# Kernel optimization log

Measured on AMD Instinct MI355X. Metric: run time of the kernel, lower is better.

The kernel has to match this reference:

```python
import jax, jax.numpy as jnp
import numpy as np

B, S, D, H, E, TOP_K = 8, 2048, 2048, 2048, 4, 2


def setup_inputs() -> dict:
    key = jax.random.key(0)
    ks = jax.random.split(key, 6)
    scale = 0.02
    return {
        "hidden_states": jax.random.normal(ks[0], (B, S, D), jnp.float32),
        "gate_w": jax.random.normal(ks[1], (E, D), jnp.float32) * scale,  # Linear(D -> E), no bias
        "w1": jax.random.normal(ks[2], (E, D, H), jnp.float32) * scale,   # per-expert Linear(D -> H)
        "b1": jnp.zeros((E, H), jnp.float32),
        "w2": jax.random.normal(ks[3], (E, H, H), jnp.float32) * scale,   # per-expert Linear(H -> H)
        "b2": jnp.zeros((E, H), jnp.float32),
    }


def reference(hidden_states, gate_w, w1, b1, w2, b2):
    b, s, d = hidden_states.shape
    x = hidden_states.reshape(-1, d)                       # [N, D]
    n = x.shape[0]

    # Router: softmax in fp32, top-k, renormalize (matches torch forward)
    logits = jnp.einsum("nd,ed->ne", x, gate_w)            # [N, E]
    rw = jax.nn.softmax(logits.astype(jnp.float32), axis=-1)
    top_w, sel = jax.lax.top_k(rw, TOP_K)                  # [N, K]
    top_w = top_w / jnp.sum(top_w, axis=-1, keepdims=True)
    top_w = top_w.astype(x.dtype)

    # Scatter top-k weights back to a dense [N, E] combine matrix
    w_full = jnp.zeros((n, E), x.dtype).at[jnp.arange(n)[:, None], sel].set(top_w)

    # Per-expert FFN: Linear -> exact GELU -> Linear (dense over all tokens,
    # combined with zero weight for unselected experts == gather/scatter math)
    h1 = jax.nn.gelu(jnp.einsum("nd,edh->enh", x, w1) + b1[:, None, :], approximate=False)
    out_e = jnp.einsum("enh,eho->eno", h1, w2) + b2[:, None, :]  # [E, N, H]

    out = jnp.einsum("eno,ne->no", out_e, w_full)          # weighted combine
    return out.reshape(b, s, -1)
```

## Files before the change

### kernel.cpp

```cpp
#include <hip/hip_runtime.h>
#include <hip/hip_bf16.h>
#include <math.h>

typedef __bf16 bf16x8 __attribute__((ext_vector_type(8)));
typedef __bf16 bf16x4 __attribute__((ext_vector_type(4)));
typedef float f32x4 __attribute__((ext_vector_type(4)));

typedef __attribute__((address_space(1))) void GV;
typedef __attribute__((address_space(3))) void LV;

template <int OSTRIDE, bool EBLOCK>
__global__ __launch_bounds__(256) void transpose_cvt(const float* __restrict__ in,
                                                     __bf16* __restrict__ out) {
  __shared__ float tile[32][33];
  const int e = blockIdx.z;
  const size_t ibase = (size_t)e * 2048 * 2048;
  const size_t obase = EBLOCK ? (size_t)e * 2048 * 2048 : (size_t)e * 2048;
  int c0 = blockIdx.x * 32, r0 = blockIdx.y * 32;
  int tx = threadIdx.x & 31, ty = threadIdx.x >> 5;
#pragma unroll
  for (int i = 0; i < 32; i += 8)
    tile[ty + i][tx] = in[ibase + (size_t)(r0 + ty + i) * 2048 + c0 + tx];
  __syncthreads();
#pragma unroll
  for (int i = 0; i < 32; i += 8)
    out[obase + (size_t)(c0 + ty + i) * OSTRIDE + r0 + tx] = (__bf16)tile[tx][ty + i];
}

__global__ __launch_bounds__(256) void router_kernel(const float* __restrict__ x,
                                                     const float* __restrict__ gw,
                                                     float* __restrict__ comb,
                                                     int* __restrict__ pairid,
                                                     int* __restrict__ cnt) {
  int lane = threadIdx.x & 63;
  int wv = threadIdx.x >> 6;
  int n = blockIdx.x * 4 + wv;
  const float* xr = x + (size_t)n * 2048;
  float s0 = 0.f, s1 = 0.f, s2 = 0.f, s3 = 0.f;
  for (int d = lane; d < 2048; d += 64) {
    float xv = xr[d];
    s0 += xv * gw[d];
    s1 += xv * gw[2048 + d];
    s2 += xv * gw[4096 + d];
    s3 += xv * gw[6144 + d];
  }
#pragma unroll
  for (int off = 32; off > 0; off >>= 1) {
    s0 += __shfl_down(s0, off);
    s1 += __shfl_down(s1, off);
    s2 += __shfl_down(s2, off);
    s3 += __shfl_down(s3, off);
  }
  if (lane == 0) {
    float l[4] = {s0, s1, s2, s3};
    float m = fmaxf(fmaxf(l[0], l[1]), fmaxf(l[2], l[3]));
    float p[4], sum = 0.f;
#pragma unroll
    for (int e = 0; e < 4; ++e) { p[e] = expf(l[e] - m); sum += p[e]; }
#pragma unroll
    for (int e = 0; e < 4; ++e) p[e] /= sum;
    int i1 = 0;
#pragma unroll
    for (int e = 1; e < 4; ++e) if (p[e] > p[i1]) i1 = e;
    int i2 = -1;
#pragma unroll
    for (int e = 0; e < 4; ++e) {
      if (e == i1) continue;
      if (i2 < 0 || p[e] > p[i2]) i2 = e;
    }
    float ws = p[i1] + p[i2];
#pragma unroll
    for (int e = 0; e < 4; ++e)
      comb[(size_t)n * 4 + e] = (e == i1 || e == i2) ? p[e] / ws : 0.f;
    int a = min(i1, i2), b = max(i1, i2);
    int pid = (a == 0) ? (b - 1) : ((a == 1) ? (1 + b) : (2 + b));
    pairid[n] = pid;
    atomicAdd(&cnt[pid], 1);
  }
}

__global__ void scan6(const int* __restrict__ cnt, int* __restrict__ off) {
  int o = 0;
  for (int i = 0; i < 6; ++i) { off[i] = o; o += cnt[i]; }
}

__global__ __launch_bounds__(256) void assign_kernel(const int* __restrict__ pairid,
                                                     const float4* __restrict__ comb4,
                                                     const int* __restrict__ off,
                                                     int* __restrict__ cur,
                                                     int* __restrict__ perm,
                                                     float4* __restrict__ comb_s,
                                                     int* __restrict__ pm_s) {
  int n = blockIdx.x * 256 + threadIdx.x;
  int pid = pairid[n];
  int pos = off[pid] + atomicAdd(&cur[pid], 1);
  perm[pos] = n;
  comb_s[pos] = comb4[n];
  const int lut[6] = {3, 5, 9, 6, 10, 12};
  pm_s[pos] = lut[pid];
}

__global__ __launch_bounds__(256) void cvt_gather(const float4* __restrict__ hs,
                                                  const int* __restrict__ perm,
                                                  bf16x4* __restrict__ xb) {
  int pos = blockIdx.x;
  int tok = perm[pos];
  const float4* src = hs + (size_t)tok * 512;
  bf16x4* dst = xb + (size_t)pos * 512;
#pragma unroll
  for (int i = 0; i < 2; ++i) {
    int j = i * 256 + threadIdx.x;
    float4 v = src[j];
    bf16x4 o;
    o.x = (__bf16)v.x; o.y = (__bf16)v.y; o.z = (__bf16)v.z; o.w = (__bf16)v.w;
    dst[j] = o;
  }
}

__global__ void tile_mask_kernel(const int* __restrict__ pm_s, int* __restrict__ tmask) {
  int t = threadIdx.x;
  int m = 0;
  for (int i = 0; i < 128; ++i) m |= pm_s[t * 128 + i];
  tmask[t] = m;
}

template <int MODE>
__global__ __launch_bounds__(256) void gemm_bt(const __bf16* __restrict__ A,
                                               const __bf16* __restrict__ Bt,
                                               const float* __restrict__ bias,
                                               const float* __restrict__ cc,
                                               const int* __restrict__ tmask,
                                               const int* __restrict__ permc,
                                               void* __restrict__ outp) {
  constexpr int K = (MODE == 0) ? 2048 : 8192;
  __shared__ __bf16 ldsA[128 * 32];
  __shared__ __bf16 ldsB[128 * 32];

  const int tid = threadIdx.x;
  const int lane = tid & 63;
  const int wv = tid >> 6;
  const int bx = blockIdx.x, by = blockIdx.y;

  const int tm = tmask[by];
  if (MODE == 0) {
    if (!(tm & (1 << (bx >> 4)))) return;
  }

  const int lrow = lane & 15;
  const int quad = lane >> 4;
  const int mbase = (wv >> 1) * 64;
  const int nbase = (wv & 1) * 64;

  f32x4 acc[4][4] = {};

  auto k_step = [&](int kb) {
    __syncthreads();
#pragma unroll
    for (int t = 0; t < 2; ++t) {
      int g = t * 256 + wv * 64 + lane;
      int row = g >> 2, kc = g & 3;
      const __bf16* ga = A + (size_t)(by * 128 + row) * K + kb * 32 + kc * 8;
      const __bf16* gb = Bt + (size_t)(bx * 128 + row) * K + kb * 32 + kc * 8;
      int loff = t * 2048 + wv * 512;
      __builtin_amdgcn_global_load_lds((GV*)ga, (LV*)&ldsA[loff], 16, 0, 0);
      __builtin_amdgcn_global_load_lds((GV*)gb, (LV*)&ldsB[loff], 16, 0, 0);
    }
    __syncthreads();

    bf16x8 af[4], bfr[4];
#pragma unroll
    for (int i = 0; i < 4; ++i)
      af[i] = *(const bf16x8*)&ldsA[(mbase + i * 16 + lrow) * 32 + quad * 8];
#pragma unroll
    for (int i = 0; i < 4; ++i)
      bfr[i] = *(const bf16x8*)&ldsB[(nbase + i * 16 + lrow) * 32 + quad * 8];
#pragma unroll
    for (int mi = 0; mi < 4; ++mi)
#pragma unroll
      for (int ni = 0; ni < 4; ++ni)
        acc[mi][ni] = __builtin_amdgcn_mfma_f32_16x16x32_bf16(af[mi], bfr[ni],
                                                              acc[mi][ni], 0, 0, 0);
  };

  if (MODE == 0) {
    for (int kb = 0; kb < K / 32; ++kb) k_step(kb);
  } else {
    for (int e = 0; e < 4; ++e) {
      if (!(tm & (1 << e))) continue;
      for (int kb = e * 64; kb < e * 64 + 64; ++kb) k_step(kb);
    }
  }

  if (MODE == 0) {
    __bf16* out = (__bf16*)outp;
#pragma unroll
    for (int mi = 0; mi < 4; ++mi) {
#pragma unroll
      for (int ni = 0; ni < 4; ++ni) {
        int gcol = bx * 128 + nbase + ni * 16 + lrow;
        int e = gcol >> 11;
        int h = gcol & 2047;
        float b = bias[e * 2048 + h];
        f32x4 v = acc[mi][ni];
#pragma unroll
        for (int r = 0; r < 4; ++r) {
          int row = by * 128 + mbase + mi * 16 + quad * 4 + r;
          float xv = v[r] + b;
          float gl = 0.5f * xv * (1.0f + erff(xv * 0.70710678118654752440f));
          out[(size_t)row * 8192 + gcol] = (__bf16)(gl * cc[row * 4 + e]);
        }
      }
    }
  } else {
    float* out = (float*)outp;
    float bb[4][4];
#pragma unroll
    for (int ni = 0; ni < 4; ++ni) {
      int gcol = bx * 128 + nbase + ni * 16 + lrow;
#pragma unroll
      for (int e = 0; e < 4; ++e) bb[ni][e] = bias[e * 2048 + gcol];
    }
#pragma unroll
    for (int mi = 0; mi < 4; ++mi) {
#pragma unroll
      for (int r = 0; r < 4; ++r) {
        int row = by * 128 + mbase + mi * 16 + quad * 4 + r;
        int tok = permc[row];
        const float* cw = cc + (size_t)row * 4;
        float c0 = cw[0], c1 = cw[1], c2 = cw[2], c3 = cw[3];
#pragma unroll
        for (int ni = 0; ni < 4; ++ni) {
          int gcol = bx * 128 + nbase + ni * 16 + lrow;
          float s = acc[mi][ni][r] + c0 * bb[ni][0] + c1 * bb[ni][1] +
                    c2 * bb[ni][2] + c3 * bb[ni][3];
          out[(size_t)tok * 2048 + gcol] = s;
        }
      }
    }
  }
}

extern "C" void kernel_launch(void* const* d_in, const int* in_sizes, int n_in,
                              void* d_out, int out_size, void* d_ws, size_t ws_size,
                              hipStream_t stream) {
  const float* hs = (const float*)d_in[0];
  const float* gate_w = (const float*)d_in[1];
  const float* w1 = (const float*)d_in[2];
  const float* b1 = (const float*)d_in[3];
  const float* w2 = (const float*)d_in[4];
  const float* b2 = (const float*)d_in[5];
  float* out = (float*)d_out;

  const int N = 16384, D = 2048, H = 2048, E = 4;
  const int CHUNK = 4096;

  char* p = (char*)d_ws;
  __bf16* xb_s = (__bf16*)p;  p += (size_t)N * D * 2;
  __bf16* w1t = (__bf16*)p;   p += (size_t)E * D * H * 2;
  __bf16* w2t = (__bf16*)p;   p += (size_t)E * H * H * 2;
  float* comb = (float*)p;    p += (size_t)N * 4 * 4;
  float* comb_s = (float*)p;  p += (size_t)N * 4 * 4;
  int* perm = (int*)p;        p += (size_t)N * 4;
  int* pairid = (int*)p;      p += (size_t)N * 4;
  int* pm_s = (int*)p;        p += (size_t)N * 4;
  int* meta = (int*)p;        p += 32 * 4;
  int* tmask = (int*)p;       p += 128 * 4;
  __bf16* h1s = (__bf16*)p;

  hipMemsetAsync(meta, 0, 64, stream);
  transpose_cvt<2048, true><<<dim3(64, 64, 4), 256, 0, stream>>>(w1, w1t);
  transpose_cvt<8192, false><<<dim3(64, 64, 4), 256, 0, stream>>>(w2, w2t);
  router_kernel<<<dim3(N / 4), 256, 0, stream>>>(hs, gate_w, comb, pairid, meta);
  scan6<<<1, 1, 0, stream>>>(meta, meta + 16);
  assign_kernel<<<dim3(N / 256), 256, 0, stream>>>(pairid, (const float4*)comb,
                                                   meta + 16, meta + 8, perm,
                                                   (float4*)comb_s, pm_s);
  cvt_gather<<<dim3(N), 256, 0, stream>>>((const float4*)hs, perm, (bf16x4*)xb_s);
  tile_mask_kernel<<<1, 128, 0, stream>>>(pm_s, tmask);

  for (int c = 0; c < N / CHUNK; ++c) {
    const __bf16* Ax = xb_s + (size_t)c * CHUNK * D;
    const float* cc = comb_s + (size_t)c * CHUNK * 4;
    const int* tmc = tmask + c * (CHUNK / 128);
    gemm_bt<0><<<dim3(E * H / 128, CHUNK / 128), 256, 0, stream>>>(Ax, w1t, b1, cc,
                                                                   tmc, nullptr, h1s);
    gemm_bt<1><<<dim3(H / 128, CHUNK / 128), 256, 0, stream>>>(h1s, w2t, b2, cc, tmc,
                                                               perm + c * CHUNK, out);
  }
}
```

Baseline: 1.698 ms.

## Fuse bf16 conversion into router and gather rows inside first GEMM

```diff
diff --git a/kernel.cpp b/kernel.cpp
--- a/kernel.cpp
+++ b/kernel.cpp
@@ -27,55 +27,72 @@
     out[obase + (size_t)(c0 + ty + i) * OSTRIDE + r0 + tx] = (__bf16)tile[tx][ty + i];
 }
 
-__global__ __launch_bounds__(256) void router_kernel(const float* __restrict__ x,
-                                                     const float* __restrict__ gw,
-                                                     float* __restrict__ comb,
-                                                     int* __restrict__ pairid,
-                                                     int* __restrict__ cnt) {
-  int lane = threadIdx.x & 63;
-  int wv = threadIdx.x >> 6;
-  int n = blockIdx.x * 4 + wv;
-  const float* xr = x + (size_t)n * 2048;
-  float s0 = 0.f, s1 = 0.f, s2 = 0.f, s3 = 0.f;
-  for (int d = lane; d < 2048; d += 64) {
-    float xv = xr[d];
-    s0 += xv * gw[d];
-    s1 += xv * gw[2048 + d];
-    s2 += xv * gw[4096 + d];
-    s3 += xv * gw[6144 + d];
-  }
-#pragma unroll
-  for (int off = 32; off > 0; off >>= 1) {
-    s0 += __shfl_down(s0, off);
-    s1 += __shfl_down(s1, off);
-    s2 += __shfl_down(s2, off);
-    s3 += __shfl_down(s3, off);
-  }
-  if (lane == 0) {
-    float l[4] = {s0, s1, s2, s3};
-    float m = fmaxf(fmaxf(l[0], l[1]), fmaxf(l[2], l[3]));
-    float p[4], sum = 0.f;
-#pragma unroll
-    for (int e = 0; e < 4; ++e) { p[e] = expf(l[e] - m); sum += p[e]; }
-#pragma unroll
-    for (int e = 0; e < 4; ++e) p[e] /= sum;
-    int i1 = 0;
-#pragma unroll
-    for (int e = 1; e < 4; ++e) if (p[e] > p[i1]) i1 = e;
-    int i2 = -1;
-#pragma unroll
-    for (int e = 0; e < 4; ++e) {
-      if (e == i1) continue;
-      if (i2 < 0 || p[e] > p[i2]) i2 = e;
-    }
-    float ws = p[i1] + p[i2];
-#pragma unroll
-    for (int e = 0; e < 4; ++e)
-      comb[(size_t)n * 4 + e] = (e == i1 || e == i2) ? p[e] / ws : 0.f;
-    int a = min(i1, i2), b = max(i1, i2);
-    int pid = (a == 0) ? (b - 1) : ((a == 1) ? (1 + b) : (2 + b));
-    pairid[n] = pid;
-    atomicAdd(&cnt[pid], 1);
+__global__ __launch_bounds__(256) void router_fused(const float4* __restrict__ hs4,
+                                                    const float4* __restrict__ gw4,
+                                                    bf16x4* __restrict__ xb,
+                                                    float* __restrict__ comb,
+                                                    int* __restrict__ pairid,
+                                                    int* __restrict__ cnt) {
+  __shared__ float4 gwS[4 * 512];
+  const int tid = threadIdx.x;
+  for (int j = tid; j < 2048; j += 256) gwS[j] = gw4[j];
+  __syncthreads();
+
+  const int lane = tid & 63;
+  const int wv = tid >> 6;
+  const int n0 = blockIdx.x * 16;
+
+  for (int t = wv; t < 16; t += 4) {
+    const int n = n0 + t;
+    const float4* xr = hs4 + (size_t)n * 512;
+    bf16x4* dst = xb + (size_t)n * 512;
+    float s0 = 0.f, s1 = 0.f, s2 = 0.f, s3 = 0.f;
+#pragma unroll
+    for (int i = 0; i < 8; ++i) {
+      int j = i * 64 + lane;
+      float4 v = xr[j];
+      float4 g0 = gwS[j], g1 = gwS[512 + j], g2 = gwS[1024 + j], g3 = gwS[1536 + j];
+      s0 += v.x * g0.x + v.y * g0.y + v.z * g0.z + v.w * g0.w;
+      s1 += v.x * g1.x + v.y * g1.y + v.z * g1.z + v.w * g1.w;
+      s2 += v.x * g2.x + v.y * g2.y + v.z * g2.z + v.w * g2.w;
+      s3 += v.x * g3.x + v.y * g3.y + v.z * g3.z + v.w * g3.w;
+      bf16x4 o;
+      o.x = (__bf16)v.x; o.y = (__bf16)v.y; o.z = (__bf16)v.z; o.w = (__bf16)v.w;
+      dst[j] = o;
+    }
+#pragma unroll
+    for (int off = 32; off > 0; off >>= 1) {
+      s0 += __shfl_down(s0, off);
+      s1 += __shfl_down(s1, off);
+      s2 += __shfl_down(s2, off);
+      s3 += __shfl_down(s3, off);
+    }
+    if (lane == 0) {
+      float l[4] = {s0, s1, s2, s3};
+      float m = fmaxf(fmaxf(l[0], l[1]), fmaxf(l[2], l[3]));
+      float p[4], sum = 0.f;
+#pragma unroll
+      for (int e = 0; e < 4; ++e) { p[e] = expf(l[e] - m); sum += p[e]; }
+#pragma unroll
+      for (int e = 0; e < 4; ++e) p[e] /= sum;
+      int i1 = 0;
+#pragma unroll
+      for (int e = 1; e < 4; ++e) if (p[e] > p[i1]) i1 = e;
+      int i2 = -1;
+#pragma unroll
+      for (int e = 0; e < 4; ++e) {
+        if (e == i1) continue;
+        if (i2 < 0 || p[e] > p[i2]) i2 = e;
+      }
+      float ws = p[i1] + p[i2];
+#pragma unroll
+      for (int e = 0; e < 4; ++e)
+        comb[(size_t)n * 4 + e] = (e == i1 || e == i2) ? p[e] / ws : 0.f;
+      int a = min(i1, i2), b = max(i1, i2);
+      int pid = (a == 0) ? (b - 1) : ((a == 1) ? (1 + b) : (2 + b));
+      pairid[n] = pid;
+      atomicAdd(&cnt[pid], 1);
+    }
   }
 }
 
@@ -100,23 +117,6 @@
   pm_s[pos] = lut[pid];
 }
 
-__global__ __launch_bounds__(256) void cvt_gather(const float4* __restrict__ hs,
-                                                  const int* __restrict__ perm,
-                                                  bf16x4* __restrict__ xb) {
-  int pos = blockIdx.x;
-  int tok = perm[pos];
-  const float4* src = hs + (size_t)tok * 512;
-  bf16x4* dst = xb + (size_t)pos * 512;
-#pragma unroll
-  for (int i = 0; i < 2; ++i) {
-    int j = i * 256 + threadIdx.x;
-    float4 v = src[j];
-    bf16x4 o;
-    o.x = (__bf16)v.x; o.y = (__bf16)v.y; o.z = (__bf16)v.z; o.w = (__bf16)v.w;
-    dst[j] = o;
-  }
-}
-
 __global__ void tile_mask_kernel(const int* __restrict__ pm_s, int* __restrict__ tmask) {
   int t = threadIdx.x;
   int m = 0;
@@ -151,16 +151,25 @@
   const int mbase = (wv >> 1) * 64;
   const int nbase = (wv & 1) * 64;
 
+  size_t aoff[2], boff[2];
+#pragma unroll
+  for (int t = 0; t < 2; ++t) {
+    int g = t * 256 + wv * 64 + lane;
+    int row = g >> 2, kc = g & 3;
+    int arow = by * 128 + row;
+    if (MODE == 0) arow = permc[arow];
+    aoff[t] = (size_t)arow * K + kc * 8;
+    boff[t] = (size_t)(bx * 128 + row) * K + kc * 8;
+  }
+
   f32x4 acc[4][4] = {};
 
   auto k_step = [&](int kb) {
     __syncthreads();
 #pragma unroll
     for (int t = 0; t < 2; ++t) {
-      int g = t * 256 + wv * 64 + lane;
-      int row = g >> 2, kc = g & 3;
-      const __bf16* ga = A + (size_t)(by * 128 + row) * K + kb * 32 + kc * 8;
-      const __bf16* gb = Bt + (size_t)(bx * 128 + row) * K + kb * 32 + kc * 8;
+      const __bf16* ga = A + aoff[t] + (size_t)kb * 32;
+      const __bf16* gb = Bt + boff[t] + (size_t)kb * 32;
       int loff = t * 2048 + wv * 512;
       __builtin_amdgcn_global_load_lds((GV*)ga, (LV*)&ldsA[loff], 16, 0, 0);
       __builtin_amdgcn_global_load_lds((GV*)gb, (LV*)&ldsB[loff], 16, 0, 0);
@@ -255,7 +264,7 @@
   const int CHUNK = 4096;
 
   char* p = (char*)d_ws;
-  __bf16* xb_s = (__bf16*)p;  p += (size_t)N * D * 2;
+  __bf16* xb = (__bf16*)p;    p += (size_t)N * D * 2;
   __bf16* w1t = (__bf16*)p;   p += (size_t)E * D * H * 2;
   __bf16* w2t = (__bf16*)p;   p += (size_t)E * H * H * 2;
   float* comb = (float*)p;    p += (size_t)N * 4 * 4;
@@ -270,20 +279,20 @@
   hipMemsetAsync(meta, 0, 64, stream);
   transpose_cvt<2048, true><<<dim3(64, 64, 4), 256, 0, stream>>>(w1, w1t);
   transpose_cvt<8192, false><<<dim3(64, 64, 4), 256, 0, stream>>>(w2, w2t);
-  router_kernel<<<dim3(N / 4), 256, 0, stream>>>(hs, gate_w, comb, pairid, meta);
+  router_fused<<<dim3(N / 16), 256, 0, stream>>>((const float4*)hs,
+                                                 (const float4*)gate_w,
+                                                 (bf16x4*)xb, comb, pairid, meta);
   scan6<<<1, 1, 0, stream>>>(meta, meta + 16);
   assign_kernel<<<dim3(N / 256), 256, 0, stream>>>(pairid, (const float4*)comb,
                                                    meta + 16, meta + 8, perm,
                                                    (float4*)comb_s, pm_s);
-  cvt_gather<<<dim3(N), 256, 0, stream>>>((const float4*)hs, perm, (bf16x4*)xb_s);
   tile_mask_kernel<<<1, 128, 0, stream>>>(pm_s, tmask);
 
   for (int c = 0; c < N / CHUNK; ++c) {
-    const __bf16* Ax = xb_s + (size_t)c * CHUNK * D;
     const float* cc = comb_s + (size_t)c * CHUNK * 4;
     const int* tmc = tmask + c * (CHUNK / 128);
-    gemm_bt<0><<<dim3(E * H / 128, CHUNK / 128), 256, 0, stream>>>(Ax, w1t, b1, cc,
-                                                                   tmc, nullptr, h1s);
+    gemm_bt<0><<<dim3(E * H / 128, CHUNK / 128), 256, 0, stream>>>(
+        xb, w1t, b1, cc, tmc, perm + c * CHUNK, h1s);
     gemm_bt<1><<<dim3(H / 128, CHUNK / 128), 256, 0, stream>>>(h1s, w2t, b2, cc, tmc,
                                                                perm + c * CHUNK, out);
   }
```

New measurement: 1.645 ms. 3.1% less time.
